# Kernel optimization log

Measured on AMD Instinct MI355X. Metric: run time of the kernel, lower is better.

Reference implementation:

```python
import jax, jax.numpy as jnp
import numpy as np

N = 50000
E = 800000
C_IN = 64
C_OUT = 64
K = 3  # Chebyshev order (num_stacks)
LAMBDA_MAX = 2.0


def setup_inputs() -> dict:
    key = jax.random.key(0)
    ks = jax.random.split(key, 32)
    inp = {
        'X': jax.random.normal(ks[0], (N, C_IN), dtype=jnp.float32),
        'edge_index': jax.random.randint(ks[1], (2, E), 0, N, dtype=jnp.int64),
        'edge_weight': jax.random.uniform(ks[2], (E,), dtype=jnp.float32),
        'H': jax.random.normal(ks[3], (N, C_OUT), dtype=jnp.float32),
        'C': jax.random.normal(ks[4], (N, C_OUT), dtype=jnp.float32),
    }
    # 8 ChebConvs: conv_{x,h}_{i,f,c,o}; x-convs map C_IN->C_OUT, h-convs C_OUT->C_OUT
    names_x = ['Wxi', 'Wxf', 'Wxc', 'Wxo']
    names_h = ['Whi', 'Whf', 'Whc', 'Who']
    i = 5
    for nx, nh in zip(names_x, names_h):
        inp[nx] = jax.random.normal(ks[i], (K, C_IN, C_OUT), dtype=jnp.float32) * (1.0 / np.sqrt(K * C_IN)); i += 1
        inp['b' + nx[1:]] = jax.random.normal(ks[i], (C_OUT,), dtype=jnp.float32) * 0.01; i += 1
        inp[nh] = jax.random.normal(ks[i], (K, C_OUT, C_OUT), dtype=jnp.float32) * (1.0 / np.sqrt(K * C_OUT)); i += 1
        inp['b' + nh[1:]] = jax.random.normal(ks[i], (C_OUT,), dtype=jnp.float32) * 0.01; i += 1
    # per-gate biases b_i, b_f, b_c, b_o of shape [1, C_OUT] (zero-initialized in torch)
    for nm in ['bi', 'bf', 'bc', 'bo']:
        inp[nm] = jax.random.normal(ks[i], (1, C_OUT), dtype=jnp.float32) * 0.01; i += 1
    return inp


def _cheb_norm(edge_index, edge_weight, n):
    # symmetric normalization: D^-1/2 W D^-1/2 (PyG get_laplacian 'sym')
    row, col = edge_index[0], edge_index[1]
    deg = jax.ops.segment_sum(edge_weight, row, num_segments=n)
    dinv = jnp.where(deg > 0, jax.lax.rsqrt(jnp.where(deg > 0, deg, 1.0)), 0.0)
    return dinv[row] * edge_weight * dinv[col]


def _cheb_conv(x, W, b, row, col, nw, n):
    # ChebConv: out = sum_k T_k(L_hat) x @ W[k] + b, with
    # L_hat v = (2/lambda_max) * (v - A_norm v) - v
    def Lhat(v):
        agg = jax.ops.segment_sum(nw[:, None] * v[col], row, num_segments=n)
        return (2.0 / LAMBDA_MAX) * (v - agg) - v
    Tx_prev = x
    out = x @ W[0]
    k = W.shape[0]
    if k > 1:
        Tx = Lhat(x)
        out = out + Tx @ W[1]
        for j in range(2, k):
            Tx_new = 2.0 * Lhat(Tx) - Tx_prev
            out = out + Tx_new @ W[j]
            Tx_prev, Tx = Tx, Tx_new
    return out + b


def reference(X, edge_index, edge_weight, H, C,
              Wxi, bxi, Whi, bhi, Wxf, bxf, Whf, bhf,
              Wxc, bxc, Whc, bhc, Wxo, bxo, Who, bho,
              bi, bf, bc, bo):
    n = X.shape[0]
    row, col = edge_index[0], edge_index[1]
    nw = _cheb_norm(edge_index, edge_weight, n)
    cc = lambda v, W, b: _cheb_conv(v, W, b, row, col, nw, n)
    I = jax.nn.sigmoid(cc(X, Wxi, bxi) + cc(H, Whi, bhi) + bi)
    F = jax.nn.sigmoid(cc(X, Wxf, bxf) + cc(H, Whf, bhf) + bf)
    T = jnp.tanh(cc(X, Wxc, bxc) + cc(H, Whc, bhc) + bc)
    C_new = F * C + I * T
    O = jax.nn.sigmoid(cc(X, Wxo, bxo) + cc(H, Who, bho) + bo)
    H_new = O * jnp.tanh(C_new)
    return (H_new, C_new)
```

## Files before the change

kernel.cpp:

```cpp
#include <hip/hip_runtime.h>

#define N_NODES 50000
#define N_PAD   50048
#define N_EDGES 800000
#define NBE4    782
#define NB_IL2  1563
#define NBKT    196
#define BCAP    4992

typedef __attribute__((ext_vector_type(8))) short bf16x8;
typedef __attribute__((ext_vector_type(4))) float f32x4;

__device__ __forceinline__ unsigned short f2bf(float f) {
    unsigned u = __float_as_uint(f);
    u = (u + 0x7fffu + ((u >> 16) & 1u)) >> 16;
    return (unsigned short)u;
}

__device__ __forceinline__ float fsig(float x) {
    x = fminf(fmaxf(x, -30.f), 30.f);
    float t = __expf(x);
    return __fdividef(t, 1.f + t);
}
__device__ __forceinline__ float ftanh(float x) {
    x = fminf(fmaxf(x, -15.f), 15.f);
    float t = __expf(2.f * x);
    return 1.f - __fdividef(2.f, t + 1.f);
}


__global__ __launch_bounds__(256) void k_prep(
    const void* __restrict__ eiraw,
    unsigned* __restrict__ hist,
    const float* __restrict__ X, const float* __restrict__ H, unsigned short* __restrict__ XH,
    const float* __restrict__ Wxi, const float* __restrict__ Whi,
    const float* __restrict__ Wxf, const float* __restrict__ Whf,
    const float* __restrict__ Wxc, const float* __restrict__ Whc,
    const float* __restrict__ Wxo, const float* __restrict__ Who,
    const float* __restrict__ bxi, const float* __restrict__ bhi,
    const float* __restrict__ bxf, const float* __restrict__ bhf,
    const float* __restrict__ bxc, const float* __restrict__ bhc,
    const float* __restrict__ bxo, const float* __restrict__ bho,
    const float* __restrict__ bgi, const float* __restrict__ bgf,
    const float* __restrict__ bgc, const float* __restrict__ bgo,
    unsigned short* __restrict__ Wf, float* __restrict__ ball) {
    __shared__ int sflag;
    __shared__ unsigned cnt[NBKT];
    int b = blockIdx.x, t = threadIdx.x;
    if (b < NBE4) {
        if (t == 0) sflag = 0;
        if (t < NBKT) cnt[t] = 0;
        __syncthreads();
        int si = b * 1024 + t;
        int sv = ((const int*)eiraw)[1 + 2 * si];
        if (sv) atomicOr(&sflag, 1);
        __syncthreads();
        int is32 = sflag;
#pragma unroll
        for (int k = 0; k < 4; k++) {
            int e = b * 1024 + k * 256 + t;
            if (e < N_EDGES) {
                int r = is32 ? ((const int*)eiraw)[e] : (int)(((const long long*)eiraw)[e]);
                atomicAdd(&cnt[r >> 8], 1u);
            }
        }
        __syncthreads();
        if (t < NBKT) hist[(size_t)t * NBE4 + b] = cnt[t];
        return;
    }
    int bb = b - NBE4;
    if (bb < NB_IL2) {
        int tt = bb * 256 + t;
        int node = tt >> 3, g = tt & 7;
        if (node >= N_NODES) return;
        const float* base = (g < 4) ? (X + (size_t)node * 64 + g * 16)
                                    : (H + (size_t)node * 64 + (g - 4) * 16);
        float4 v0 = ((const float4*)base)[0];
        float4 v1 = ((const float4*)base)[1];
        float4 v2 = ((const float4*)base)[2];
        float4 v3 = ((const float4*)base)[3];
        uint4 o0, o1;
        o0.x = (unsigned)f2bf(v0.x) | ((unsigned)f2bf(v0.y) << 16);
        o0.y = (unsigned)f2bf(v0.z) | ((unsigned)f2bf(v0.w) << 16);
        o0.z = (unsigned)f2bf(v1.x) | ((unsigned)f2bf(v1.y) << 16);
        o0.w = (unsigned)f2bf(v1.z) | ((unsigned)f2bf(v1.w) << 16);
        o1.x = (unsigned)f2bf(v2.x) | ((unsigned)f2bf(v2.y) << 16);
        o1.y = (unsigned)f2bf(v2.z) | ((unsigned)f2bf(v2.w) << 16);
        o1.z = (unsigned)f2bf(v3.x) | ((unsigned)f2bf(v3.y) << 16);
        o1.w = (unsigned)f2bf(v3.z) | ((unsigned)f2bf(v3.w) << 16);
        unsigned short* dst = XH + (size_t)node * 128 + g * 16;
        *(uint4*)dst = o0;
        *(uint4*)(dst + 8) = o1;
        return;
    }
    bb -= NB_IL2;
    if (bb < 48) {
        int flat = bb * 256 + t;
        int l = flat & 63, nt = (flat >> 6) & 15, ks = flat >> 10;
        int n = nt * 16 + (l & 15);
        int g = n >> 6, c = n & 63;
        const float* WX = (g == 0) ? Wxi : (g == 1) ? Wxf : (g == 2) ? Wxc : Wxo;
        const float* WH = (g == 0) ? Whi : (g == 1) ? Whf : (g == 2) ? Whc : Who;
        int k0 = ks * 32 + (l >> 4) * 8;
        unsigned short ov[8];
#pragma unroll
        for (int j = 0; j < 8; j++) {
            int k = k0 + j;
            int bsel = k >> 7, ch = k & 127;
            const float* W = (ch < 64) ? WX : WH;
            int kk = ch & 63;
            float v;
            if (bsel == 0)      v = W[kk * 64 + c] - W[2 * 4096 + kk * 64 + c];
            else if (bsel == 1) v = -W[4096 + kk * 64 + c];
            else                v = 2.f * W[2 * 4096 + kk * 64 + c];
            ov[j] = f2bf(v);
        }
        uint4 o;
        o.x = (unsigned)ov[0] | ((unsigned)ov[1] << 16);
        o.y = (unsigned)ov[2] | ((unsigned)ov[3] << 16);
        o.z = (unsigned)ov[4] | ((unsigned)ov[5] << 16);
        o.w = (unsigned)ov[6] | ((unsigned)ov[7] << 16);
        *(uint4*)(Wf + (size_t)flat * 8) = o;
    } else {
        int g = t >> 6, c = t & 63;
        const float* BX = (g == 0) ? bxi : (g == 1) ? bxf : (g == 2) ? bxc : bxo;
        const float* BH = (g == 0) ? bhi : (g == 1) ? bhf : (g == 2) ? bhc : bho;
        const float* BG = (g == 0) ? bgi : (g == 1) ? bgf : (g == 2) ? bgc : bgo;
        ball[t] = BX[c] + BH[c] + BG[c];
    }
}


__global__ __launch_bounds__(256) void k_bscan(unsigned* __restrict__ hist, unsigned* __restrict__ btot) {
    __shared__ unsigned s[256];
    int j = blockIdx.x, t = threadIdx.x;
    unsigned* row = hist + (size_t)j * NBE4;
    unsigned v[4];
#pragma unroll
    for (int k = 0; k < 4; k++) {
        int i = t * 4 + k;
        v[k] = (i < NBE4) ? row[i] : 0u;
    }
    unsigned tsum = v[0] + v[1] + v[2] + v[3];
    s[t] = tsum; __syncthreads();
    for (int d = 1; d < 256; d <<= 1) {
        unsigned a = (t >= d) ? s[t - d] : 0u;
        __syncthreads();
        s[t] += a;
        __syncthreads();
    }
    unsigned run = s[t] - tsum;
#pragma unroll
    for (int k = 0; k < 4; k++) {
        int i = t * 4 + k;
        if (i < NBE4) { unsigned c = v[k]; row[i] = run; run += c; }
    }
    if (t == 255) btot[j] = s[255];
}


__global__ __launch_bounds__(256) void k_scat(const void* __restrict__ eiraw, const float* __restrict__ w,
                                              const unsigned* __restrict__ hist, const unsigned* __restrict__ btot,
                                              unsigned long long* __restrict__ ebuf) {
    __shared__ int sflag;
    __shared__ unsigned ssc[256];
    __shared__ unsigned boff[NBKT];
    __shared__ unsigned cur[NBKT];
    int b = blockIdx.x, t = threadIdx.x;
    unsigned v = (t < NBKT) ? btot[t] : 0u;
    ssc[t] = v; __syncthreads();
    for (int d = 1; d < 256; d <<= 1) {
        unsigned a = (t >= d) ? ssc[t - d] : 0u;
        __syncthreads();
        ssc[t] += a;
        __syncthreads();
    }
    if (t < NBKT) { boff[t] = (ssc[t] - v) + hist[(size_t)t * NBE4 + b]; cur[t] = 0u; }
    if (t == 0) sflag = 0;
    __syncthreads();
    int si = b * 1024 + t;
    int sv = ((const int*)eiraw)[1 + 2 * si];
    if (sv) atomicOr(&sflag, 1);
    __syncthreads();
    int is32 = sflag;
#pragma unroll
    for (int k = 0; k < 4; k++) {
        int e = b * 1024 + k * 256 + t;
        if (e < N_EDGES) {
            int r, c;
            if (is32) { r = ((const int*)eiraw)[e]; c = ((const int*)eiraw)[N_EDGES + e]; }
            else      { r = (int)(((const long long*)eiraw)[e]); c = (int)(((const long long*)eiraw)[N_EDGES + e]); }
            float wv = w[e];
            int bk = r >> 8;
            unsigned lr = atomicAdd(&cur[bk], 1u);
            unsigned pos = boff[bk] + lr;
            ebuf[pos] = ((unsigned long long)(unsigned)r << 48)
                      | (((unsigned long long)(unsigned)c & 0xffffull) << 32)
                      | (unsigned long long)__float_as_uint(wv);
        }
    }
}


__global__ __launch_bounds__(1024) void k_build(const unsigned long long* __restrict__ ebuf,
                                                const unsigned* __restrict__ btot,
                                                int* __restrict__ rp, float* __restrict__ dinv,
                                                int* __restrict__ colp, float* __restrict__ wraw) {
    __shared__ unsigned long long se[BCAP];
    __shared__ unsigned ssc[256];
    __shared__ unsigned cnt[256];
    __shared__ float wsum[256];
    __shared__ unsigned off[256];
    __shared__ unsigned cur[256];
    int b = blockIdx.x, t = threadIdx.x;
    if (t < 256) ssc[t] = (t < NBKT) ? btot[t] : 0u;
    __syncthreads();
    for (int d = 1; d < 256; d <<= 1) {
        unsigned a = 0u;
        if (t < 256 && t >= d) a = ssc[t - d];
        __syncthreads();
        if (t < 256) ssc[t] += a;
        __syncthreads();
    }
    unsigned base = (b > 0) ? ssc[b - 1] : 0u;
    unsigned end  = ssc[b];
    int n = (int)(end - base);
    if (b == 0 && t == 0) rp[N_NODES] = N_EDGES;
    if (t < 256) { cnt[t] = 0u; wsum[t] = 0.f; }
    __syncthreads();
    for (int i = t; i < n; i += 1024) {
        unsigned long long e = ebuf[base + i];
        if (i < BCAP) se[i] = e;
        unsigned lr = (unsigned)(e >> 48) & 255u;
        atomicAdd(&cnt[lr], 1u);
        atomicAdd(&wsum[lr], __uint_as_float((unsigned)(e & 0xffffffffu)));
    }
    __syncthreads();
    if (t < 256) off[t] = cnt[t];
    __syncthreads();
    for (int d = 1; d < 256; d <<= 1) {
        unsigned a = 0u;
        if (t < 256 && t >= d) a = off[t - d];
        __syncthreads();
        if (t < 256) off[t] += a;
        __syncthreads();
    }
    if (t < 256) {
        unsigned excl = off[t] - cnt[t];
        off[t] = excl;
        cur[t] = excl;
        int row = b * 256 + t;
        if (row < N_NODES) {
            rp[row] = (int)(base + excl);
            float dg = wsum[t];
            dinv[row] = (dg > 0.f) ? rsqrtf(dg) : 0.f;
        }
    }
    __syncthreads();
    for (int i = t; i < n; i += 1024) {
        unsigned long long e = (i < BCAP) ? se[i] : ebuf[base + i];
        unsigned lr = (unsigned)(e >> 48) & 255u;
        unsigned p = atomicAdd(&cur[lr], 1u);
        int row = b * 256 + (int)lr;
        int c = (int)((e >> 32) & 0xffffu);
        colp[base + p] = (row << 16) | c;
        wraw[base + p] = __uint_as_float((unsigned)(e & 0xffffffffu));
    }
}


__global__ __launch_bounds__(256) void k_nw(const int* __restrict__ colp, const float* __restrict__ wraw,
                                            const float* __restrict__ dinv, int2* __restrict__ cw) {
    int e = blockIdx.x * 256 + threadIdx.x;
    if (e >= N_EDGES) return;
    unsigned rc = (unsigned)colp[e];
    int c = (int)(rc & 0xffffu);
    float nw = dinv[rc >> 16] * wraw[e] * dinv[c];
    cw[e] = make_int2(c, __float_as_int(nw));
}


__global__ __launch_bounds__(256) void k_spmv_bf(const unsigned short* __restrict__ src,
                                                 unsigned short* __restrict__ dst,
                                                 const int* __restrict__ rp,
                                                 const int2* __restrict__ cw) {
    int wid = threadIdx.x >> 6, lane = threadIdx.x & 63;
    int node = blockIdx.x * 4 + wid;
    if (node >= N_NODES) return;
    int s = rp[node], e = rp[node + 1];
    float a0 = 0.f, a1 = 0.f;
    for (int jb = s; jb < e; jb += 8) {
        int2 cv[8]; unsigned vv[8];
#pragma unroll
        for (int k = 0; k < 8; k++) {
            int j = jb + k;
            int jc = (j < e) ? j : (e - 1);
            cv[k] = cw[jc];
            if (j >= e) cv[k].y = 0;
        }
#pragma unroll
        for (int k = 0; k < 8; k++)
            vv[k] = *(const unsigned*)(src + (size_t)cv[k].x * 128 + lane * 2);
#pragma unroll
        for (int k = 0; k < 8; k++) {
            float wv = __int_as_float(cv[k].y);
            a0 = fmaf(wv, __uint_as_float(vv[k] << 16), a0);
            a1 = fmaf(wv, __uint_as_float(vv[k] & 0xffff0000u), a1);
        }
    }
    unsigned o = (unsigned)f2bf(a0) | ((unsigned)f2bf(a1) << 16);
    *(unsigned*)(dst + (size_t)node * 128 + lane * 2) = o;
}


__global__ __launch_bounds__(256) void k_gemm_mfma(
    const unsigned short* __restrict__ XH, const unsigned short* __restrict__ U1,
    const unsigned short* __restrict__ U2, const unsigned short* __restrict__ Wf,
    const float* __restrict__ ball, const float* __restrict__ C, float* __restrict__ out) {
    __shared__ __align__(16) uint4 Bs[2][1024];

    int t = threadIdx.x;
    int wid = t >> 6, lane = t & 63;
    int col = lane & 15, quad = lane >> 4;
    int m0 = blockIdx.x * 64 + wid * 16;
    int arow = m0 + col;

    f32x4 acc[16];
#pragma unroll
    for (int i = 0; i < 16; i++) acc[i] = (f32x4){0.f, 0.f, 0.f, 0.f};

    const unsigned short* srcs[3] = {XH, U1, U2};

    bf16x8 a_cur = *(const bf16x8*)(srcs[0] + (size_t)arow * 128 + quad * 8);
    const uint4* g0 = (const uint4*)Wf;
    uint4 p0 = g0[t], p1 = g0[t + 256], p2 = g0[t + 512], p3 = g0[t + 768];

    for (int ks = 0; ks < 12; ks++) {
        uint4* dstb = Bs[ks & 1];
        dstb[t] = p0; dstb[t + 256] = p1; dstb[t + 512] = p2; dstb[t + 768] = p3;
        __syncthreads();
        bf16x8 a_nxt = a_cur;
        if (ks < 11) {
            int ks1 = ks + 1;
            const uint4* g = (const uint4*)(Wf + (size_t)ks1 * 8192);
            p0 = g[t]; p1 = g[t + 256]; p2 = g[t + 512]; p3 = g[t + 768];
            a_nxt = *(const bf16x8*)(srcs[ks1 >> 2] + (size_t)arow * 128 + (ks1 & 3) * 32 + quad * 8);
        }
        const unsigned short* B = (const unsigned short*)Bs[ks & 1];
#pragma unroll
        for (int nt = 0; nt < 16; nt++) {
            bf16x8 bfrag = *(const bf16x8*)(B + nt * 512 + lane * 8);
            acc[nt] = __builtin_amdgcn_mfma_f32_16x16x32_bf16(a_cur, bfrag, acc[nt], 0, 0, 0);
        }
        a_cur = a_nxt;
    }

    float bI[4], bF[4], bT[4], bO[4];
#pragma unroll
    for (int cq = 0; cq < 4; cq++) {
        int c = cq * 16 + col;
        bI[cq] = ball[c]; bF[cq] = ball[64 + c]; bT[cq] = ball[128 + c]; bO[cq] = ball[192 + c];
    }
#pragma unroll
    for (int r = 0; r < 4; r++) {
        int node = m0 + quad * 4 + r;
        if (node >= N_NODES) continue;
#pragma unroll
        for (int cq = 0; cq < 4; cq++) {
            int c = cq * 16 + col;
            float ig = fsig(acc[0 + cq][r]  + bI[cq]);
            float fg = fsig(acc[4 + cq][r]  + bF[cq]);
            float tg = ftanh(acc[8 + cq][r] + bT[cq]);
            float og = fsig(acc[12 + cq][r] + bO[cq]);
            float cv = fmaf(fg, C[(size_t)node * 64 + c], ig * tg);
            out[(size_t)node * 64 + c] = og * ftanh(cv);
            out[(size_t)N_NODES * 64 + (size_t)node * 64 + c] = cv;
        }
    }
}


extern "C" void kernel_launch(void* const* d_in, const int* in_sizes, int n_in,
                              void* d_out, int out_size, void* d_ws, size_t ws_size,
                              hipStream_t stream) {
    const float* X   = (const float*)d_in[0];
    const void*  ei  = d_in[1];
    const float* w   = (const float*)d_in[2];
    const float* H   = (const float*)d_in[3];
    const float* C   = (const float*)d_in[4];
    const float* Wxi = (const float*)d_in[5];  const float* bxi = (const float*)d_in[6];
    const float* Whi = (const float*)d_in[7];  const float* bhi = (const float*)d_in[8];
    const float* Wxf = (const float*)d_in[9];  const float* bxf = (const float*)d_in[10];
    const float* Whf = (const float*)d_in[11]; const float* bhf = (const float*)d_in[12];
    const float* Whc = (const float*)d_in[15]; const float* bxc_ = (const float*)d_in[14];
    const float* Wxc = (const float*)d_in[13];
    const float* bhc = (const float*)d_in[16];
    const float* Wxo = (const float*)d_in[17]; const float* bxo = (const float*)d_in[18];
    const float* Who = (const float*)d_in[19]; const float* bho = (const float*)d_in[20];
    const float* bgi = (const float*)d_in[21]; const float* bgf = (const float*)d_in[22];
    const float* bgc = (const float*)d_in[23]; const float* bgo = (const float*)d_in[24];
    const float* bxc = bxc_;
    float* out = (float*)d_out;

    char* ws = (char*)d_ws;
    size_t off = 0;
    auto alloc = [&](size_t bytes) -> char* {
        char* p = ws + off;
        off = (off + bytes + 255) & ~(size_t)255;
        return p;
    };
    unsigned* hist  = (unsigned*)alloc((size_t)NBKT * NBE4 * 4);
    unsigned* btot  = (unsigned*)alloc((NBKT + 1) * 4);
    unsigned long long* ebuf = (unsigned long long*)alloc((size_t)N_EDGES * 8);
    int*   rp   = (int*)alloc((N_NODES + 1) * 4);
    float* dinv = (float*)alloc(N_NODES * 4);
    int*   colp = (int*)alloc((size_t)(N_EDGES + 8) * 4);
    float* wraw = (float*)alloc((size_t)(N_EDGES + 8) * 4);
    int2*  cw   = (int2*)alloc((size_t)(N_EDGES + 16) * 8);
    unsigned short* XH = (unsigned short*)alloc((size_t)N_PAD * 128 * 2);
    unsigned short* U1 = (unsigned short*)alloc((size_t)N_PAD * 128 * 2);
    unsigned short* U2 = (unsigned short*)alloc((size_t)N_PAD * 128 * 2);
    unsigned short* Wf = (unsigned short*)alloc((size_t)12 * 16 * 64 * 8 * 2);
    float* ball = (float*)alloc(256 * 4);
    (void)ws_size; (void)in_sizes; (void)n_in; (void)out_size;

    k_prep<<<NBE4 + NB_IL2 + 49, 256, 0, stream>>>(ei, hist, X, H, XH,
                                                   Wxi, Whi, Wxf, Whf, Wxc, Whc, Wxo, Who,
                                                   bxi, bhi, bxf, bhf, bxc, bhc, bxo, bho,
                                                   bgi, bgf, bgc, bgo, Wf, ball);
    k_bscan<<<NBKT, 256, 0, stream>>>(hist, btot);
    k_scat<<<NBE4, 256, 0, stream>>>(ei, w, hist, btot, ebuf);
    k_build<<<NBKT, 1024, 0, stream>>>(ebuf, btot, rp, dinv, colp, wraw);
    k_nw<<<(N_EDGES + 255) / 256, 256, 0, stream>>>(colp, wraw, dinv, cw);
    k_spmv_bf<<<(N_NODES + 3) / 4, 256, 0, stream>>>(XH, U1, rp, cw);
    k_spmv_bf<<<(N_NODES + 3) / 4, 256, 0, stream>>>(U1, U2, rp, cw);
    k_gemm_mfma<<<(N_NODES + 63) / 64, 256, 0, stream>>>(XH, U1, U2, Wf, ball, C, out);
}
```

Baseline: 288.8 us.

## Fuse CSR build preprocessing into one cooperative kernel with grid syncs

Merges the prep, bucket-scan, scatter, build and normalization kernels into a single cooperative kernel of 196 blocks of 1024 threads, using grid.sync between phases in place of separate launches. It also drops the colp/wraw intermediates by writing row-scaled weights straight into cw, and moves the column-side dinv multiply into the SpMV as an extra gather. This removes several launch gaps and a pass over the edges. In exchange, parallelism in the histogram and convert phases falls to 196 blocks, and every SpMV edge now does an additional dinv load.

```diff
diff --git a/kernel.cpp b/kernel.cpp
--- a/kernel.cpp
+++ b/kernel.cpp
@@ -1,11 +1,13 @@
 #include <hip/hip_runtime.h>
+#include <hip/hip_cooperative_groups.h>
+
+namespace cg = cooperative_groups;
 
 #define N_NODES 50000
 #define N_PAD   50048
 #define N_EDGES 800000
-#define NBE4    782
-#define NB_IL2  1563
 #define NBKT    196
+#define ESPAN   4096
 #define BCAP    4992
 
 typedef __attribute__((ext_vector_type(8))) short bf16x8;
@@ -29,52 +31,57 @@
 }
 
 
-__global__ __launch_bounds__(256) void k_prep(
-    const void* __restrict__ eiraw,
-    unsigned* __restrict__ hist,
-    const float* __restrict__ X, const float* __restrict__ H, unsigned short* __restrict__ XH,
-    const float* __restrict__ Wxi, const float* __restrict__ Whi,
-    const float* __restrict__ Wxf, const float* __restrict__ Whf,
-    const float* __restrict__ Wxc, const float* __restrict__ Whc,
-    const float* __restrict__ Wxo, const float* __restrict__ Who,
-    const float* __restrict__ bxi, const float* __restrict__ bhi,
-    const float* __restrict__ bxf, const float* __restrict__ bhf,
-    const float* __restrict__ bxc, const float* __restrict__ bhc,
-    const float* __restrict__ bxo, const float* __restrict__ bho,
-    const float* __restrict__ bgi, const float* __restrict__ bgf,
-    const float* __restrict__ bgc, const float* __restrict__ bgo,
-    unsigned short* __restrict__ Wf, float* __restrict__ ball) {
-    __shared__ int sflag;
-    __shared__ unsigned cnt[NBKT];
+struct FrontArgs {
+    const void* eiraw; const float* w;
+    const float* X; const float* H; unsigned short* XH;
+    unsigned* hist; unsigned* btot;
+    unsigned long long* ebuf;
+    int* rp; float* dinv; int2* cw;
+    const float* Wxi; const float* Whi; const float* Wxf; const float* Whf;
+    const float* Wxc; const float* Whc; const float* Wxo; const float* Who;
+    const float* bxi; const float* bhi; const float* bxf; const float* bhf;
+    const float* bxc; const float* bhc; const float* bxo; const float* bho;
+    const float* bgi; const float* bgf; const float* bgc; const float* bgo;
+    unsigned short* Wf; float* ball;
+};
+
+__global__ __launch_bounds__(1024) void k_front(FrontArgs a) {
+    __shared__ unsigned long long se[BCAP];
+    __shared__ unsigned s0[256];
+    __shared__ unsigned cnt[256];
+    __shared__ float    fsum[256];
+    __shared__ unsigned cur[256];
+    __shared__ unsigned boff[256];
+    __shared__ float    dloc[256];
+    __shared__ int      sflag;
+
+    cg::grid_group grid = cg::this_grid();
     int b = blockIdx.x, t = threadIdx.x;
-    if (b < NBE4) {
-        if (t == 0) sflag = 0;
-        if (t < NBKT) cnt[t] = 0;
-        __syncthreads();
-        int si = b * 1024 + t;
-        int sv = ((const int*)eiraw)[1 + 2 * si];
+    int flat = b * 1024 + t;
+    int e0 = b * ESPAN;
+    int e1 = (e0 + ESPAN < N_EDGES) ? e0 + ESPAN : N_EDGES;
+
+    if (t == 0) sflag = 0;
+    if (t < NBKT) cnt[t] = 0u;
+    __syncthreads();
+    if (e0 + t < e1) {
+        int sv = ((const int*)a.eiraw)[1 + 2 * (e0 + t)];
         if (sv) atomicOr(&sflag, 1);
-        __syncthreads();
-        int is32 = sflag;
-#pragma unroll
-        for (int k = 0; k < 4; k++) {
-            int e = b * 1024 + k * 256 + t;
-            if (e < N_EDGES) {
-                int r = is32 ? ((const int*)eiraw)[e] : (int)(((const long long*)eiraw)[e]);
-                atomicAdd(&cnt[r >> 8], 1u);
-            }
-        }
-        __syncthreads();
-        if (t < NBKT) hist[(size_t)t * NBE4 + b] = cnt[t];
-        return;
-    }
-    int bb = b - NBE4;
-    if (bb < NB_IL2) {
-        int tt = bb * 256 + t;
-        int node = tt >> 3, g = tt & 7;
-        if (node >= N_NODES) return;
-        const float* base = (g < 4) ? (X + (size_t)node * 64 + g * 16)
-                                    : (H + (size_t)node * 64 + (g - 4) * 16);
+    }
+    __syncthreads();
+    int is32 = sflag;
+
+    for (int e = e0 + t; e < e1; e += 1024) {
+        int r = is32 ? ((const int*)a.eiraw)[e] : (int)(((const long long*)a.eiraw)[e]);
+        atomicAdd(&cnt[r >> 8], 1u);
+    }
+    __syncthreads();
+    if (t < NBKT) a.hist[(size_t)t * NBKT + b] = cnt[t];
+
+    for (int u = flat; u < N_NODES * 8; u += NBKT * 1024) {
+        int node = u >> 3, g = u & 7;
+        const float* base = (g < 4) ? (a.X + (size_t)node * 64 + g * 16)
+                                    : (a.H + (size_t)node * 64 + (g - 4) * 16);
         float4 v0 = ((const float4*)base)[0];
         float4 v1 = ((const float4*)base)[1];
         float4 v2 = ((const float4*)base)[2];
@@ -88,19 +95,17 @@
         o1.y = (unsigned)f2bf(v2.z) | ((unsigned)f2bf(v2.w) << 16);
         o1.z = (unsigned)f2bf(v3.x) | ((unsigned)f2bf(v3.y) << 16);
         o1.w = (unsigned)f2bf(v3.z) | ((unsigned)f2bf(v3.w) << 16);
-        unsigned short* dst = XH + (size_t)node * 128 + g * 16;
+        unsigned short* dst = a.XH + (size_t)node * 128 + g * 16;
         *(uint4*)dst = o0;
         *(uint4*)(dst + 8) = o1;
-        return;
-    }
-    bb -= NB_IL2;
-    if (bb < 48) {
-        int flat = bb * 256 + t;
+    }
+
+    if (flat < 12288) {
         int l = flat & 63, nt = (flat >> 6) & 15, ks = flat >> 10;
         int n = nt * 16 + (l & 15);
         int g = n >> 6, c = n & 63;
-        const float* WX = (g == 0) ? Wxi : (g == 1) ? Wxf : (g == 2) ? Wxc : Wxo;
-        const float* WH = (g == 0) ? Whi : (g == 1) ? Whf : (g == 2) ? Whc : Who;
+        const float* WX = (g == 0) ? a.Wxi : (g == 1) ? a.Wxf : (g == 2) ? a.Wxc : a.Wxo;
+        const float* WH = (g == 0) ? a.Whi : (g == 1) ? a.Whf : (g == 2) ? a.Whc : a.Who;
         int k0 = ks * 32 + (l >> 4) * 8;
         unsigned short ov[8];
 #pragma unroll
@@ -120,177 +125,129 @@
         o.y = (unsigned)ov[2] | ((unsigned)ov[3] << 16);
         o.z = (unsigned)ov[4] | ((unsigned)ov[5] << 16);
         o.w = (unsigned)ov[6] | ((unsigned)ov[7] << 16);
-        *(uint4*)(Wf + (size_t)flat * 8) = o;
-    } else {
-        int g = t >> 6, c = t & 63;
-        const float* BX = (g == 0) ? bxi : (g == 1) ? bxf : (g == 2) ? bxc : bxo;
-        const float* BH = (g == 0) ? bhi : (g == 1) ? bhf : (g == 2) ? bhc : bho;
-        const float* BG = (g == 0) ? bgi : (g == 1) ? bgf : (g == 2) ? bgc : bgo;
-        ball[t] = BX[c] + BH[c] + BG[c];
-    }
-}
-
-
-__global__ __launch_bounds__(256) void k_bscan(unsigned* __restrict__ hist, unsigned* __restrict__ btot) {
-    __shared__ unsigned s[256];
-    int j = blockIdx.x, t = threadIdx.x;
-    unsigned* row = hist + (size_t)j * NBE4;
-    unsigned v[4];
-#pragma unroll
-    for (int k = 0; k < 4; k++) {
-        int i = t * 4 + k;
-        v[k] = (i < NBE4) ? row[i] : 0u;
-    }
-    unsigned tsum = v[0] + v[1] + v[2] + v[3];
-    s[t] = tsum; __syncthreads();
-    for (int d = 1; d < 256; d <<= 1) {
-        unsigned a = (t >= d) ? s[t - d] : 0u;
-        __syncthreads();
-        s[t] += a;
-        __syncthreads();
-    }
-    unsigned run = s[t] - tsum;
-#pragma unroll
-    for (int k = 0; k < 4; k++) {
-        int i = t * 4 + k;
-        if (i < NBE4) { unsigned c = v[k]; row[i] = run; run += c; }
-    }
-    if (t == 255) btot[j] = s[255];
-}
-
-
-__global__ __launch_bounds__(256) void k_scat(const void* __restrict__ eiraw, const float* __restrict__ w,
-                                              const unsigned* __restrict__ hist, const unsigned* __restrict__ btot,
-                                              unsigned long long* __restrict__ ebuf) {
-    __shared__ int sflag;
-    __shared__ unsigned ssc[256];
-    __shared__ unsigned boff[NBKT];
-    __shared__ unsigned cur[NBKT];
-    int b = blockIdx.x, t = threadIdx.x;
-    unsigned v = (t < NBKT) ? btot[t] : 0u;
-    ssc[t] = v; __syncthreads();
-    for (int d = 1; d < 256; d <<= 1) {
-        unsigned a = (t >= d) ? ssc[t - d] : 0u;
-        __syncthreads();
-        ssc[t] += a;
-        __syncthreads();
-    }
-    if (t < NBKT) { boff[t] = (ssc[t] - v) + hist[(size_t)t * NBE4 + b]; cur[t] = 0u; }
-    if (t == 0) sflag = 0;
-    __syncthreads();
-    int si = b * 1024 + t;
-    int sv = ((const int*)eiraw)[1 + 2 * si];
-    if (sv) atomicOr(&sflag, 1);
-    __syncthreads();
-    int is32 = sflag;
-#pragma unroll
-    for (int k = 0; k < 4; k++) {
-        int e = b * 1024 + k * 256 + t;
-        if (e < N_EDGES) {
+        *(uint4*)(a.Wf + (size_t)flat * 8) = o;
+    } else if (flat < 12544) {
+        int tt = flat - 12288;
+        int g = tt >> 6, c = tt & 63;
+        const float* BX = (g == 0) ? a.bxi : (g == 1) ? a.bxf : (g == 2) ? a.bxc : a.bxo;
+        const float* BH = (g == 0) ? a.bhi : (g == 1) ? a.bhf : (g == 2) ? a.bhc : a.bho;
+        const float* BG = (g == 0) ? a.bgi : (g == 1) ? a.bgf : (g == 2) ? a.bgc : a.bgo;
+        a.ball[tt] = BX[c] + BH[c] + BG[c];
+    }
+    grid.sync();
+
+    {
+        unsigned* row = a.hist + (size_t)b * NBKT;
+        unsigned v = (t < NBKT) ? row[t] : 0u;
+        if (t < 256) s0[t] = v;
+        __syncthreads();
+        for (int d = 1; d < 256; d <<= 1) {
+            unsigned x = 0u;
+            if (t < 256 && t >= d) x = s0[t - d];
+            __syncthreads();
+            if (t < 256) s0[t] += x;
+            __syncthreads();
+        }
+        if (t < NBKT) row[t] = s0[t] - v;
+        if (t == 0) a.btot[b] = s0[255];
+    }
+    grid.sync();
+
+    {
+        unsigned v = (t < NBKT) ? a.btot[t] : 0u;
+        if (t < 256) s0[t] = v;
+        __syncthreads();
+        for (int d = 1; d < 256; d <<= 1) {
+            unsigned x = 0u;
+            if (t < 256 && t >= d) x = s0[t - d];
+            __syncthreads();
+            if (t < 256) s0[t] += x;
+            __syncthreads();
+        }
+        if (t < NBKT) { boff[t] = (s0[t] - v) + a.hist[(size_t)t * NBKT + b]; cur[t] = 0u; }
+        __syncthreads();
+        for (int e = e0 + t; e < e1; e += 1024) {
             int r, c;
-            if (is32) { r = ((const int*)eiraw)[e]; c = ((const int*)eiraw)[N_EDGES + e]; }
-            else      { r = (int)(((const long long*)eiraw)[e]); c = (int)(((const long long*)eiraw)[N_EDGES + e]); }
-            float wv = w[e];
+            if (is32) { r = ((const int*)a.eiraw)[e]; c = ((const int*)a.eiraw)[N_EDGES + e]; }
+            else      { r = (int)(((const long long*)a.eiraw)[e]); c = (int)(((const long long*)a.eiraw)[N_EDGES + e]); }
+            float wv = a.w[e];
             int bk = r >> 8;
             unsigned lr = atomicAdd(&cur[bk], 1u);
-            unsigned pos = boff[bk] + lr;
-            ebuf[pos] = ((unsigned long long)(unsigned)r << 48)
-                      | (((unsigned long long)(unsigned)c & 0xffffull) << 32)
-                      | (unsigned long long)__float_as_uint(wv);
-        }
-    }
-}
-
-
-__global__ __launch_bounds__(1024) void k_build(const unsigned long long* __restrict__ ebuf,
-                                                const unsigned* __restrict__ btot,
-                                                int* __restrict__ rp, float* __restrict__ dinv,
-                                                int* __restrict__ colp, float* __restrict__ wraw) {
-    __shared__ unsigned long long se[BCAP];
-    __shared__ unsigned ssc[256];
-    __shared__ unsigned cnt[256];
-    __shared__ float wsum[256];
-    __shared__ unsigned off[256];
-    __shared__ unsigned cur[256];
-    int b = blockIdx.x, t = threadIdx.x;
-    if (t < 256) ssc[t] = (t < NBKT) ? btot[t] : 0u;
-    __syncthreads();
-    for (int d = 1; d < 256; d <<= 1) {
-        unsigned a = 0u;
-        if (t < 256 && t >= d) a = ssc[t - d];
-        __syncthreads();
-        if (t < 256) ssc[t] += a;
-        __syncthreads();
-    }
-    unsigned base = (b > 0) ? ssc[b - 1] : 0u;
-    unsigned end  = ssc[b];
-    int n = (int)(end - base);
-    if (b == 0 && t == 0) rp[N_NODES] = N_EDGES;
-    if (t < 256) { cnt[t] = 0u; wsum[t] = 0.f; }
-    __syncthreads();
-    for (int i = t; i < n; i += 1024) {
-        unsigned long long e = ebuf[base + i];
-        if (i < BCAP) se[i] = e;
-        unsigned lr = (unsigned)(e >> 48) & 255u;
-        atomicAdd(&cnt[lr], 1u);
-        atomicAdd(&wsum[lr], __uint_as_float((unsigned)(e & 0xffffffffu)));
-    }
-    __syncthreads();
-    if (t < 256) off[t] = cnt[t];
-    __syncthreads();
-    for (int d = 1; d < 256; d <<= 1) {
-        unsigned a = 0u;
-        if (t < 256 && t >= d) a = off[t - d];
-        __syncthreads();
-        if (t < 256) off[t] += a;
-        __syncthreads();
-    }
-    if (t < 256) {
-        unsigned excl = off[t] - cnt[t];
-        off[t] = excl;
-        cur[t] = excl;
-        int row = b * 256 + t;
-        if (row < N_NODES) {
-            rp[row] = (int)(base + excl);
-            float dg = wsum[t];
-            dinv[row] = (dg > 0.f) ? rsqrtf(dg) : 0.f;
-        }
-    }
-    __syncthreads();
-    for (int i = t; i < n; i += 1024) {
-        unsigned long long e = (i < BCAP) ? se[i] : ebuf[base + i];
-        unsigned lr = (unsigned)(e >> 48) & 255u;
-        unsigned p = atomicAdd(&cur[lr], 1u);
-        int row = b * 256 + (int)lr;
-        int c = (int)((e >> 32) & 0xffffu);
-        colp[base + p] = (row << 16) | c;
-        wraw[base + p] = __uint_as_float((unsigned)(e & 0xffffffffu));
-    }
-}
-
-
-__global__ __launch_bounds__(256) void k_nw(const int* __restrict__ colp, const float* __restrict__ wraw,
-                                            const float* __restrict__ dinv, int2* __restrict__ cw) {
-    int e = blockIdx.x * 256 + threadIdx.x;
-    if (e >= N_EDGES) return;
-    unsigned rc = (unsigned)colp[e];
-    int c = (int)(rc & 0xffffu);
-    float nw = dinv[rc >> 16] * wraw[e] * dinv[c];
-    cw[e] = make_int2(c, __float_as_int(nw));
+            a.ebuf[boff[bk] + lr] = ((unsigned long long)(unsigned)r << 48)
+                                  | (((unsigned long long)(unsigned)c & 0xffffull) << 32)
+                                  | (unsigned long long)__float_as_uint(wv);
+        }
+    }
+    grid.sync();
+
+    {
+        unsigned v = (t < NBKT) ? a.btot[t] : 0u;
+        if (t < 256) s0[t] = v;
+        __syncthreads();
+        for (int d = 1; d < 256; d <<= 1) {
+            unsigned x = 0u;
+            if (t < 256 && t >= d) x = s0[t - d];
+            __syncthreads();
+            if (t < 256) s0[t] += x;
+            __syncthreads();
+        }
+        unsigned base = (b > 0) ? s0[b - 1] : 0u;
+        unsigned end  = s0[b];
+        int n = (int)(end - base);
+        if (b == 0 && t == 0) a.rp[N_NODES] = N_EDGES;
+        if (t < 256) { cnt[t] = 0u; fsum[t] = 0.f; }
+        __syncthreads();
+        for (int i = t; i < n; i += 1024) {
+            unsigned long long e = a.ebuf[base + i];
+            if (i < BCAP) se[i] = e;
+            unsigned lr = (unsigned)(e >> 48) & 255u;
+            atomicAdd(&cnt[lr], 1u);
+            atomicAdd(&fsum[lr], __uint_as_float((unsigned)(e & 0xffffffffu)));
+        }
+        __syncthreads();
+        if (t < 256) s0[t] = cnt[t];
+        __syncthreads();
+        for (int d = 1; d < 256; d <<= 1) {
+            unsigned x = 0u;
+            if (t < 256 && t >= d) x = s0[t - d];
+            __syncthreads();
+            if (t < 256) s0[t] += x;
+            __syncthreads();
+        }
+        if (t < 256) {
+            unsigned excl = s0[t] - cnt[t];
+            cur[t] = excl;
+            float dg = fsum[t];
+            float dv = (dg > 0.f) ? rsqrtf(dg) : 0.f;
+            dloc[t] = dv;
+            int row = b * 256 + t;
+            if (row < N_NODES) { a.rp[row] = (int)(base + excl); a.dinv[row] = dv; }
+        }
+        __syncthreads();
+        for (int i = t; i < n; i += 1024) {
+            unsigned long long e = (i < BCAP) ? se[i] : a.ebuf[base + i];
+            unsigned lr = (unsigned)(e >> 48) & 255u;
+            unsigned p = atomicAdd(&cur[lr], 1u);
+            int c = (int)((e >> 32) & 0xffffu);
+            float wd = __uint_as_float((unsigned)(e & 0xffffffffu)) * dloc[lr];
+            a.cw[base + p] = make_int2(c, __float_as_int(wd));
+        }
+    }
 }
 
 
 __global__ __launch_bounds__(256) void k_spmv_bf(const unsigned short* __restrict__ src,
                                                  unsigned short* __restrict__ dst,
                                                  const int* __restrict__ rp,
-                                                 const int2* __restrict__ cw) {
+                                                 const int2* __restrict__ cw,
+                                                 const float* __restrict__ dinv) {
     int wid = threadIdx.x >> 6, lane = threadIdx.x & 63;
     int node = blockIdx.x * 4 + wid;
     if (node >= N_NODES) return;
     int s = rp[node], e = rp[node + 1];
     float a0 = 0.f, a1 = 0.f;
     for (int jb = s; jb < e; jb += 8) {
-        int2 cv[8]; unsigned vv[8];
+        int2 cv[8]; float dv[8]; unsigned vv[8];
 #pragma unroll
         for (int k = 0; k < 8; k++) {
             int j = jb + k;
@@ -300,10 +257,13 @@
         }
 #pragma unroll
         for (int k = 0; k < 8; k++)
+            dv[k] = dinv[cv[k].x];
+#pragma unroll
+        for (int k = 0; k < 8; k++)
             vv[k] = *(const unsigned*)(src + (size_t)cv[k].x * 128 + lane * 2);
 #pragma unroll
         for (int k = 0; k < 8; k++) {
-            float wv = __int_as_float(cv[k].y);
+            float wv = __int_as_float(cv[k].y) * dv[k];
             a0 = fmaf(wv, __uint_as_float(vv[k] << 16), a0);
             a1 = fmaf(wv, __uint_as_float(vv[k] & 0xffff0000u), a1);
         }
@@ -392,14 +352,12 @@
     const float* Whi = (const float*)d_in[7];  const float* bhi = (const float*)d_in[8];
     const float* Wxf = (const float*)d_in[9];  const float* bxf = (const float*)d_in[10];
     const float* Whf = (const float*)d_in[11]; const float* bhf = (const float*)d_in[12];
-    const float* Whc = (const float*)d_in[15]; const float* bxc_ = (const float*)d_in[14];
-    const float* Wxc = (const float*)d_in[13];
-    const float* bhc = (const float*)d_in[16];
+    const float* Wxc = (const float*)d_in[13]; const float* bxc = (const float*)d_in[14];
+    const float* Whc = (const float*)d_in[15]; const float* bhc = (const float*)d_in[16];
     const float* Wxo = (const float*)d_in[17]; const float* bxo = (const float*)d_in[18];
     const float* Who = (const float*)d_in[19]; const float* bho = (const float*)d_in[20];
     const float* bgi = (const float*)d_in[21]; const float* bgf = (const float*)d_in[22];
     const float* bgc = (const float*)d_in[23]; const float* bgo = (const float*)d_in[24];
-    const float* bxc = bxc_;
     float* out = (float*)d_out;
 
     char* ws = (char*)d_ws;
@@ -409,13 +367,11 @@
         off = (off + bytes + 255) & ~(size_t)255;
         return p;
     };
-    unsigned* hist  = (unsigned*)alloc((size_t)NBKT * NBE4 * 4);
+    unsigned* hist  = (unsigned*)alloc((size_t)NBKT * NBKT * 4);
     unsigned* btot  = (unsigned*)alloc((NBKT + 1) * 4);
     unsigned long long* ebuf = (unsigned long long*)alloc((size_t)N_EDGES * 8);
     int*   rp   = (int*)alloc((N_NODES + 1) * 4);
     float* dinv = (float*)alloc(N_NODES * 4);
-    int*   colp = (int*)alloc((size_t)(N_EDGES + 8) * 4);
-    float* wraw = (float*)alloc((size_t)(N_EDGES + 8) * 4);
     int2*  cw   = (int2*)alloc((size_t)(N_EDGES + 16) * 8);
     unsigned short* XH = (unsigned short*)alloc((size_t)N_PAD * 128 * 2);
     unsigned short* U1 = (unsigned short*)alloc((size_t)N_PAD * 128 * 2);
@@ -424,15 +380,20 @@
     float* ball = (float*)alloc(256 * 4);
     (void)ws_size; (void)in_sizes; (void)n_in; (void)out_size;
 
-    k_prep<<<NBE4 + NB_IL2 + 49, 256, 0, stream>>>(ei, hist, X, H, XH,
-                                                   Wxi, Whi, Wxf, Whf, Wxc, Whc, Wxo, Who,
-                                                   bxi, bhi, bxf, bhf, bxc, bhc, bxo, bho,
-                                                   bgi, bgf, bgc, bgo, Wf, ball);
-    k_bscan<<<NBKT, 256, 0, stream>>>(hist, btot);
-    k_scat<<<NBE4, 256, 0, stream>>>(ei, w, hist, btot, ebuf);
-    k_build<<<NBKT, 1024, 0, stream>>>(ebuf, btot, rp, dinv, colp, wraw);
-    k_nw<<<(N_EDGES + 255) / 256, 256, 0, stream>>>(colp, wraw, dinv, cw);
-    k_spmv_bf<<<(N_NODES + 3) / 4, 256, 0, stream>>>(XH, U1, rp, cw);
-    k_spmv_bf<<<(N_NODES + 3) / 4, 256, 0, stream>>>(U1, U2, rp, cw);
+    FrontArgs fa;
+    fa.eiraw = ei; fa.w = w; fa.X = X; fa.H = H; fa.XH = XH;
+    fa.hist = hist; fa.btot = btot; fa.ebuf = ebuf;
+    fa.rp = rp; fa.dinv = dinv; fa.cw = cw;
+    fa.Wxi = Wxi; fa.Whi = Whi; fa.Wxf = Wxf; fa.Whf = Whf;
+    fa.Wxc = Wxc; fa.Whc = Whc; fa.Wxo = Wxo; fa.Who = Who;
+    fa.bxi = bxi; fa.bhi = bhi; fa.bxf = bxf; fa.bhf = bhf;
+    fa.bxc = bxc; fa.bhc = bhc; fa.bxo = bxo; fa.bho = bho;
+    fa.bgi = bgi; fa.bgf = bgf; fa.bgc = bgc; fa.bgo = bgo;
+    fa.Wf = Wf; fa.ball = ball;
+    void* kargs[] = { &fa };
+    hipLaunchCooperativeKernel((void*)k_front, dim3(NBKT), dim3(1024), kargs, 0u, stream);
+
+    k_spmv_bf<<<(N_NODES + 3) / 4, 256, 0, stream>>>(XH, U1, rp, cw, dinv);
+    k_spmv_bf<<<(N_NODES + 3) / 4, 256, 0, stream>>>(U1, U2, rp, cw, dinv);
     k_gemm_mfma<<<(N_NODES + 63) / 64, 256, 0, stream>>>(XH, U1, U2, Wf, ball, C, out);
 }
```

Result: slower. 407.7 us (+41.2%).
